# Kernel optimization log

Measured on AMD Instinct MI355X. Metric: run time of the kernel, lower is better.

The kernel has to match this reference:

```python
import jax, jax.numpy as jnp
import numpy as np

B, T, D, H = 1024, 256, 128, 64

def setup_inputs() -> dict:
    key = jax.random.key(0)
    ks = jax.random.split(key, 9)
    s = 1.0 / np.sqrt(H)  # PyTorch LSTM init scale
    x = jax.random.normal(ks[0], (B, T, D), dtype=jnp.float32)
    W_ih = jax.random.uniform(ks[1], (4 * H, D), dtype=jnp.float32, minval=-s, maxval=s)
    W_hh = jax.random.uniform(ks[2], (4 * H, H), dtype=jnp.float32, minval=-s, maxval=s)
    b_ih = jax.random.uniform(ks[3], (4 * H,), dtype=jnp.float32, minval=-s, maxval=s)
    b_hh = jax.random.uniform(ks[4], (4 * H,), dtype=jnp.float32, minval=-s, maxval=s)
    W1 = jax.random.uniform(ks[5], (32, H), dtype=jnp.float32, minval=-s, maxval=s)
    b1 = jax.random.uniform(ks[6], (32,), dtype=jnp.float32, minval=-s, maxval=s)
    W2 = jax.random.uniform(ks[7], (1, 32), dtype=jnp.float32, minval=-0.18, maxval=0.18)
    b2 = jax.random.uniform(ks[8], (1,), dtype=jnp.float32, minval=-0.18, maxval=0.18)
    return {"x": x, "W_ih": W_ih, "W_hh": W_hh, "b_ih": b_ih, "b_hh": b_hh,
            "W1": W1, "b1": b1, "W2": W2, "b2": b2}

def reference(x, W_ih, W_hh, b_ih, b_hh, W1, b1, W2, b2):
    b = b_ih + b_hh
    # Precompute input-to-hidden projections for all timesteps: [B,T,4H]
    x_proj = jnp.einsum('btd,gd->btg', x, W_ih) + b

    def step(carry, xp_t):
        h, c = carry
        gates = xp_t + h @ W_hh.T  # [B,4H]
        i, f, g, o = jnp.split(gates, 4, axis=-1)  # PyTorch gate order
        i = jax.nn.sigmoid(i)
        f = jax.nn.sigmoid(f)
        g = jnp.tanh(g)
        o = jax.nn.sigmoid(o)
        c = f * c + i * g
        h = o * jnp.tanh(c)
        return (h, c), None

    h0 = jnp.zeros((x.shape[0], H), dtype=x.dtype)
    c0 = jnp.zeros((x.shape[0], H), dtype=x.dtype)
    (h, _), _ = jax.lax.scan(step, (h0, c0), jnp.swapaxes(x_proj, 0, 1))  # scan over T

    y = jax.nn.relu(h @ W1.T + b1)  # [B,32]
    y = jax.nn.sigmoid(y @ W2.T + b2)  # [B,1]
    return y.reshape(-1)
```

## Files before the change

kernel.cpp:

```cpp
#include <hip/hip_runtime.h>
#include <math.h>

constexpr int B_ = 1024;
constexpr int T_ = 256;
constexpr int D_ = 128;
constexpr int H_ = 64;
constexpr int G_ = 256;
constexpr int M_ = B_ * T_;

typedef short     v8s __attribute__((ext_vector_type(8)));
typedef float     v4f __attribute__((ext_vector_type(4)));
typedef _Float16  h2  __attribute__((ext_vector_type(2)));

__device__ __forceinline__ float sigmoidf_(float x) {
    return 1.0f / (1.0f + __expf(-x));
}
__device__ __forceinline__ float tanhf_(float x) {
    return fmaf(2.0f, 1.0f / (1.0f + __expf(-2.0f * x)), -1.0f);
}
__device__ __forceinline__ unsigned short f2bf(float f) {
    unsigned u = __float_as_uint(f);
    u = (u + 0x7fffu + ((u >> 16) & 1u)) >> 16;
    return (unsigned short)u;
}
__device__ __forceinline__ v8s pack8(float4 a, float4 b) {
    v8s r;
    r[0] = (short)f2bf(a.x); r[1] = (short)f2bf(a.y);
    r[2] = (short)f2bf(a.z); r[3] = (short)f2bf(a.w);
    r[4] = (short)f2bf(b.x); r[5] = (short)f2bf(b.y);
    r[6] = (short)f2bf(b.z); r[7] = (short)f2bf(b.w);
    return r;
}
__device__ __forceinline__ unsigned pkh2(float a, float b) {
    h2 v; v[0] = (_Float16)a; v[1] = (_Float16)b;
    return __builtin_bit_cast(unsigned, v);
}
__device__ __forceinline__ float fdot2_(unsigned a, unsigned b, float c) {
#if __has_builtin(__builtin_amdgcn_fdot2)
    return __builtin_amdgcn_fdot2(__builtin_bit_cast(h2, a),
                                  __builtin_bit_cast(h2, b), c, false);
#else
    h2 ha = __builtin_bit_cast(h2, a), hb = __builtin_bit_cast(h2, b);
    return c + (float)ha[0] * (float)hb[0] + (float)ha[1] * (float)hb[1];
#endif
}

__global__ __launch_bounds__(256, 2)
void xproj_f16_kernel(const float* __restrict__ x,
                      const float* __restrict__ W_ih,
                      const float* __restrict__ b_ih,
                      const float* __restrict__ b_hh,
                      unsigned short* __restrict__ xp)
{
    const int tch  = blockIdx.x;
    const int bblk = blockIdx.y;
    const int tid  = threadIdx.x;
    const int wv   = tid >> 6;
    const int lane = tid & 63;
    const int q    = lane >> 4;
    const int ml   = lane & 15;

    __shared__ __align__(16) unsigned short xs[16][136];
    __shared__ __align__(16) unsigned short tbuf[16][272];

    v8s afr[4][4];
    v4f bias[4];
    #pragma unroll
    for (int cls = 0; cls < 4; ++cls) {
        const int gr = (cls * 4 + wv) * 16 + ml;
        #pragma unroll
        for (int ks = 0; ks < 4; ++ks) {
            const float* p = W_ih + (size_t)gr * D_ + ks * 32 + q * 8;
            afr[cls][ks] = pack8(((const float4*)p)[0], ((const float4*)p)[1]);
        }
        #pragma unroll
        for (int r = 0; r < 4; ++r) {
            const int g2 = (cls * 4 + wv) * 16 + q * 4 + r;
            bias[cls][r] = b_ih[g2] + b_hh[g2];
        }
    }

    for (int tl = 0; tl < 16; ++tl) {
        const int t = tch * 16 + tl;

        #pragma unroll
        for (int i = 0; i < 2; ++i) {
            int f4  = tid + i * 256;
            int row = f4 >> 5, c4 = f4 & 31;
            float4 v = ((const float4*)(x + ((size_t)(bblk * 16 + row) * T_
                                             + t) * D_))[c4];
            short4 s;
            s.x = (short)f2bf(v.x); s.y = (short)f2bf(v.y);
            s.z = (short)f2bf(v.z); s.w = (short)f2bf(v.w);
            *(short4*)&xs[row][c4 * 4] = s;
        }
        __syncthreads();

        v4f acc[4];
        #pragma unroll
        for (int cls = 0; cls < 4; ++cls) acc[cls] = bias[cls];
        #pragma unroll
        for (int ks = 0; ks < 4; ++ks) {
            v8s bf = *(const v8s*)&xs[ml][ks * 32 + q * 8];
            #pragma unroll
            for (int cls = 0; cls < 4; ++cls)
                acc[cls] = __builtin_amdgcn_mfma_f32_16x16x32_bf16(
                    afr[cls][ks], bf, acc[cls], 0, 0, 0);
        }

        #pragma unroll
        for (int cls = 0; cls < 4; ++cls) {
            uint2 pk;
            pk.x = pkh2(acc[cls][0], acc[cls][1]);
            pk.y = pkh2(acc[cls][2], acc[cls][3]);
            *(uint2*)&tbuf[ml][cls * 64 + wv * 16 + q * 4] = pk;
        }
        __syncthreads();

        {
            const int br = tid >> 4, seg = tid & 15;
            uint4 r0 = *(const uint4*)&tbuf[br][seg * 16];
            uint4 r1 = *(const uint4*)&tbuf[br][seg * 16 + 8];
            unsigned short* orow = xp + ((size_t)(bblk * 16 + br) * T_ + t) * G_
                                      + seg * 16;
            *(uint4*)orow       = r0;
            *(uint4*)(orow + 8) = r1;
        }
    }
}

__global__ __launch_bounds__(256, 4)
void rec_dot2_kernel(const unsigned short* __restrict__ xp,
                     const float* __restrict__ W_hh,
                     const float* __restrict__ W1,
                     const float* __restrict__ b1,
                     const float* __restrict__ W2,
                     const float* __restrict__ b2,
                     float* __restrict__ out)
{
    const int b   = blockIdx.x;
    const int g   = threadIdx.x;
    const int cls = g >> 6;

    __shared__ __align__(16) unsigned hbuf[2][32];
    __shared__ float gates[G_];
    __shared__ float hf[H_];
    __shared__ float ys[32];

    uint4 wp[8];
    #pragma unroll
    for (int k8 = 0; k8 < 8; ++k8) {
        const float* p = W_hh + (size_t)g * H_ + k8 * 8;
        float4 v0 = ((const float4*)p)[0];
        float4 v1 = ((const float4*)p)[1];
        wp[k8].x = pkh2(v0.x, v0.y);
        wp[k8].y = pkh2(v0.z, v0.w);
        wp[k8].z = pkh2(v1.x, v1.y);
        wp[k8].w = pkh2(v1.z, v1.w);
    }

    if (g < 32) hbuf[0][g] = 0u;
    float c = 0.0f, hval = 0.0f;

    const unsigned short* __restrict__ xrow = xp + (size_t)b * T_ * G_ + g;
    unsigned short xv = xrow[0];
    __syncthreads();

    for (int t = 0; t < T_; ++t) {
        const int par = t & 1;
        unsigned short xn = xrow[(size_t)((t + 1 < T_) ? t + 1 : T_ - 1) * G_];

        float a0 = 0.f, a1 = 0.f, a2 = 0.f, a3 = 0.f;
        const uint4* hb = (const uint4*)hbuf[par];
        #pragma unroll
        for (int k8 = 0; k8 < 8; ++k8) {
            uint4 hv = hb[k8];
            a0 = fdot2_(wp[k8].x, hv.x, a0);
            a1 = fdot2_(wp[k8].y, hv.y, a1);
            a2 = fdot2_(wp[k8].z, hv.z, a2);
            a3 = fdot2_(wp[k8].w, hv.w, a3);
        }
        float pre = (float)__builtin_bit_cast(_Float16, xv)
                  + ((a0 + a1) + (a2 + a3));
        gates[g] = (cls == 2) ? tanhf_(pre) : sigmoidf_(pre);
        __syncthreads();

        if (g < H_) {
            float gi = gates[g];
            float gf = gates[H_ + g];
            float gg = gates[2 * H_ + g];
            float go = gates[3 * H_ + g];
            c    = fmaf(gf, c, gi * gg);
            hval = go * tanhf_(c);
            ((_Float16*)hbuf[1 - par])[g] = (_Float16)hval;
        }
        __syncthreads();
        xv = xn;
    }

    if (g < H_) hf[g] = hval;
    __syncthreads();
    if (g < 32) {
        float acc = b1[g];
        const float4* w1r = (const float4*)(W1 + (size_t)g * H_);
        #pragma unroll
        for (int k4 = 0; k4 < 16; ++k4) {
            float4 h4 = *(const float4*)&hf[k4 * 4];
            float4 w4 = w1r[k4];
            acc = fmaf(w4.x, h4.x, acc); acc = fmaf(w4.y, h4.y, acc);
            acc = fmaf(w4.z, h4.z, acc); acc = fmaf(w4.w, h4.w, acc);
        }
        ys[g] = fmaxf(acc, 0.0f);
    }
    __syncthreads();
    if (g == 0) {
        float acc = b2[0];
        #pragma unroll
        for (int j = 0; j < 32; ++j) acc = fmaf(W2[j], ys[j], acc);
        out[b] = sigmoidf_(acc);
    }
}

__global__ __launch_bounds__(256, 2)
void lstm_fused_kernel(const float* __restrict__ x,
                       const float* __restrict__ W_ih,
                       const float* __restrict__ W_hh,
                       const float* __restrict__ b_ih,
                       const float* __restrict__ b_hh,
                       const float* __restrict__ W1,
                       const float* __restrict__ b1,
                       const float* __restrict__ W2,
                       const float* __restrict__ b2,
                       float* __restrict__ out)
{
    const int b = blockIdx.x;
    const int g = threadIdx.x;

    __shared__ __align__(16) float xs[D_];
    __shared__ __align__(16) float hs[H_];
    __shared__ __align__(16) float gts[G_];
    __shared__ __align__(16) float yss[32];

    float wih[D_];
    float whhr[H_];
    {
        const float4* wr = (const float4*)(W_ih + (size_t)g * D_);
        #pragma unroll
        for (int k = 0; k < D_ / 4; ++k) {
            float4 v = wr[k];
            wih[4*k+0] = v.x; wih[4*k+1] = v.y;
            wih[4*k+2] = v.z; wih[4*k+3] = v.w;
        }
    }
    {
        const float4* wr = (const float4*)(W_hh + (size_t)g * H_);
        #pragma unroll
        for (int k = 0; k < H_ / 4; ++k) {
            float4 v = wr[k];
            whhr[4*k+0] = v.x; whhr[4*k+1] = v.y;
            whhr[4*k+2] = v.z; whhr[4*k+3] = v.w;
        }
    }
    const float bg  = b_ih[g] + b_hh[g];
    const int   cls = g >> 6;

    float c = 0.0f;
    if (g < H_) hs[g] = 0.0f;

    const float* __restrict__ xrow = x + (size_t)b * T_ * D_;

    for (int t = 0; t < T_; ++t) {
        if (g < D_) xs[g] = xrow[(size_t)t * D_ + g];
        __syncthreads();

        float a0 = bg, a1 = 0.f, a2 = 0.f, a3 = 0.f;
        const float4* xs4 = (const float4*)xs;
        #pragma unroll
        for (int k = 0; k < D_ / 4; ++k) {
            float4 v = xs4[k];
            a0 = fmaf(wih[4*k+0], v.x, a0);
            a1 = fmaf(wih[4*k+1], v.y, a1);
            a2 = fmaf(wih[4*k+2], v.z, a2);
            a3 = fmaf(wih[4*k+3], v.w, a3);
        }
        const float4* hs4 = (const float4*)hs;
        #pragma unroll
        for (int k = 0; k < H_ / 4; ++k) {
            float4 v = hs4[k];
            a0 = fmaf(whhr[4*k+0], v.x, a0);
            a1 = fmaf(whhr[4*k+1], v.y, a1);
            a2 = fmaf(whhr[4*k+2], v.z, a2);
            a3 = fmaf(whhr[4*k+3], v.w, a3);
        }
        float acc = (a0 + a1) + (a2 + a3);
        gts[g] = (cls == 2) ? tanhf_(acc) : sigmoidf_(acc);
        __syncthreads();

        if (g < H_) {
            float gi = gts[g];
            float gf = gts[H_ + g];
            float gg = gts[2 * H_ + g];
            float go = gts[3 * H_ + g];
            c = fmaf(gf, c, gi * gg);
            hs[g] = go * tanhf_(c);
        }
    }
    __syncthreads();

    if (g < 32) {
        float acc = b1[g];
        const float* w1r = W1 + g * H_;
        #pragma unroll
        for (int k = 0; k < H_; ++k) acc = fmaf(w1r[k], hs[k], acc);
        yss[g] = fmaxf(acc, 0.0f);
    }
    __syncthreads();
    if (g == 0) {
        float acc = b2[0];
        #pragma unroll
        for (int k = 0; k < 32; ++k) acc = fmaf(W2[k], yss[k], acc);
        out[b] = sigmoidf_(acc);
    }
}

extern "C" void kernel_launch(void* const* d_in, const int* in_sizes, int n_in,
                              void* d_out, int out_size, void* d_ws, size_t ws_size,
                              hipStream_t stream) {
    const float* x    = (const float*)d_in[0];
    const float* W_ih = (const float*)d_in[1];
    const float* W_hh = (const float*)d_in[2];
    const float* b_ih = (const float*)d_in[3];
    const float* b_hh = (const float*)d_in[4];
    const float* W1   = (const float*)d_in[5];
    const float* b1   = (const float*)d_in[6];
    const float* W2   = (const float*)d_in[7];
    const float* b2   = (const float*)d_in[8];
    float* out = (float*)d_out;

    const size_t xp_bytes = (size_t)M_ * G_ * sizeof(unsigned short);

    if (ws_size >= xp_bytes) {
        unsigned short* xp = (unsigned short*)d_ws;
        xproj_f16_kernel<<<dim3(16, 64), dim3(256), 0, stream>>>(
            x, W_ih, b_ih, b_hh, xp);
        rec_dot2_kernel<<<dim3(B_), dim3(256), 0, stream>>>(
            xp, W_hh, W1, b1, W2, b2, out);
    } else {
        lstm_fused_kernel<<<dim3(B_), dim3(256), 0, stream>>>(
            x, W_ih, W_hh, b_ih, b_hh, W1, b1, W2, b2, out);
    }
}
```

Baseline: 405.4 us.

## Run LSTM recurrence in a single wavefront per batch row, removing block barriers

The recurrent kernel now uses one 64-lane wavefront per batch element. Each lane computes all four gates for its hidden unit, holding four rows of W_hh packed as fp16 in registers. This removes the shared gate buffer and the two __syncthreads per timestep, which are replaced by an LDS waitcnt inside the single wave. In exchange each lane does four times the dot-product work per step, and register pressure rises enough to cut occupancy. The design also leans on lockstep execution within the wave for the shared h exchange.

```diff
diff --git a/kernel.cpp b/kernel.cpp
--- a/kernel.cpp
+++ b/kernel.cpp
@@ -129,8 +129,8 @@
     }
 }
 
-__global__ __launch_bounds__(256, 4)
-void rec_dot2_kernel(const unsigned short* __restrict__ xp,
+__global__ __launch_bounds__(64, 1)
+void rec_wave_kernel(const unsigned short* __restrict__ xp,
                      const float* __restrict__ W_hh,
                      const float* __restrict__ W1,
                      const float* __restrict__ b1,
@@ -138,71 +138,81 @@
                      const float* __restrict__ b2,
                      float* __restrict__ out)
 {
-    const int b   = blockIdx.x;
-    const int g   = threadIdx.x;
-    const int cls = g >> 6;
-
-    __shared__ __align__(16) unsigned hbuf[2][32];
-    __shared__ float gates[G_];
+    const int b    = blockIdx.x;
+    const int lane = threadIdx.x;
+
+    __shared__ __align__(16) unsigned hb[2][32];
     __shared__ float hf[H_];
     __shared__ float ys[32];
 
-    uint4 wp[8];
+    uint4 wp[4][8];
     #pragma unroll
-    for (int k8 = 0; k8 < 8; ++k8) {
-        const float* p = W_hh + (size_t)g * H_ + k8 * 8;
-        float4 v0 = ((const float4*)p)[0];
-        float4 v1 = ((const float4*)p)[1];
-        wp[k8].x = pkh2(v0.x, v0.y);
-        wp[k8].y = pkh2(v0.z, v0.w);
-        wp[k8].z = pkh2(v1.x, v1.y);
-        wp[k8].w = pkh2(v1.z, v1.w);
-    }
-
-    if (g < 32) hbuf[0][g] = 0u;
+    for (int r = 0; r < 4; ++r) {
+        const float* p = W_hh + (size_t)(r * H_ * 4 + lane) * H_ / 4;
+        p = W_hh + (size_t)(r * 64 + lane) * H_;
+        #pragma unroll
+        for (int k8 = 0; k8 < 8; ++k8) {
+            float4 v0 = ((const float4*)(p + k8 * 8))[0];
+            float4 v1 = ((const float4*)(p + k8 * 8))[1];
+            wp[r][k8].x = pkh2(v0.x, v0.y);
+            wp[r][k8].y = pkh2(v0.z, v0.w);
+            wp[r][k8].z = pkh2(v1.x, v1.y);
+            wp[r][k8].w = pkh2(v1.z, v1.w);
+        }
+    }
+
+    if (lane < 32) { hb[0][lane] = 0u; hb[1][lane] = 0u; }
     float c = 0.0f, hval = 0.0f;
 
-    const unsigned short* __restrict__ xrow = xp + (size_t)b * T_ * G_ + g;
-    unsigned short xv = xrow[0];
+    const unsigned short* __restrict__ xptr = xp + (size_t)b * T_ * G_ + lane;
+    unsigned short xv0 = xptr[0],   xv1 = xptr[64];
+    unsigned short xv2 = xptr[128], xv3 = xptr[192];
     __syncthreads();
 
     for (int t = 0; t < T_; ++t) {
+        const unsigned short* xnp =
+            xptr + (size_t)((t + 1 < T_) ? t + 1 : T_ - 1) * G_;
+        unsigned short xn0 = xnp[0],   xn1 = xnp[64];
+        unsigned short xn2 = xnp[128], xn3 = xnp[192];
+
         const int par = t & 1;
-        unsigned short xn = xrow[(size_t)((t + 1 < T_) ? t + 1 : T_ - 1) * G_];
-
-        float a0 = 0.f, a1 = 0.f, a2 = 0.f, a3 = 0.f;
-        const uint4* hb = (const uint4*)hbuf[par];
+        const uint4* hb4 = (const uint4*)hb[par];
+        float a0[4] = {0.f, 0.f, 0.f, 0.f};
+        float a1[4] = {0.f, 0.f, 0.f, 0.f};
         #pragma unroll
         for (int k8 = 0; k8 < 8; ++k8) {
-            uint4 hv = hb[k8];
-            a0 = fdot2_(wp[k8].x, hv.x, a0);
-            a1 = fdot2_(wp[k8].y, hv.y, a1);
-            a2 = fdot2_(wp[k8].z, hv.z, a2);
-            a3 = fdot2_(wp[k8].w, hv.w, a3);
-        }
-        float pre = (float)__builtin_bit_cast(_Float16, xv)
-                  + ((a0 + a1) + (a2 + a3));
-        gates[g] = (cls == 2) ? tanhf_(pre) : sigmoidf_(pre);
-        __syncthreads();
-
-        if (g < H_) {
-            float gi = gates[g];
-            float gf = gates[H_ + g];
-            float gg = gates[2 * H_ + g];
-            float go = gates[3 * H_ + g];
-            c    = fmaf(gf, c, gi * gg);
-            hval = go * tanhf_(c);
-            ((_Float16*)hbuf[1 - par])[g] = (_Float16)hval;
-        }
-        __syncthreads();
-        xv = xn;
-    }
-
-    if (g < H_) hf[g] = hval;
-    __syncthreads();
-    if (g < 32) {
-        float acc = b1[g];
-        const float4* w1r = (const float4*)(W1 + (size_t)g * H_);
+            uint4 hv = hb4[k8];
+            #pragma unroll
+            for (int r = 0; r < 4; ++r) {
+                a0[r] = fdot2_(wp[r][k8].x, hv.x, a0[r]);
+                a1[r] = fdot2_(wp[r][k8].y, hv.y, a1[r]);
+                a0[r] = fdot2_(wp[r][k8].z, hv.z, a0[r]);
+                a1[r] = fdot2_(wp[r][k8].w, hv.w, a1[r]);
+            }
+        }
+        float pre0 = (float)__builtin_bit_cast(_Float16, xv0) + (a0[0] + a1[0]);
+        float pre1 = (float)__builtin_bit_cast(_Float16, xv1) + (a0[1] + a1[1]);
+        float pre2 = (float)__builtin_bit_cast(_Float16, xv2) + (a0[2] + a1[2]);
+        float pre3 = (float)__builtin_bit_cast(_Float16, xv3) + (a0[3] + a1[3]);
+
+        float gi = sigmoidf_(pre0);
+        float gf = sigmoidf_(pre1);
+        float gg = tanhf_(pre2);
+        float go = sigmoidf_(pre3);
+        c    = fmaf(gf, c, gi * gg);
+        hval = go * tanhf_(c);
+
+        ((_Float16*)hb[par ^ 1])[lane] = (_Float16)hval;
+        asm volatile("s_waitcnt lgkmcnt(0)" ::: "memory");
+
+        xv0 = xn0; xv1 = xn1; xv2 = xn2; xv3 = xn3;
+    }
+
+    hf[lane] = hval;
+    __syncthreads();
+    if (lane < 32) {
+        float acc = b1[lane];
+        const float4* w1r = (const float4*)(W1 + (size_t)lane * H_);
         #pragma unroll
         for (int k4 = 0; k4 < 16; ++k4) {
             float4 h4 = *(const float4*)&hf[k4 * 4];
@@ -210,10 +220,10 @@
             acc = fmaf(w4.x, h4.x, acc); acc = fmaf(w4.y, h4.y, acc);
             acc = fmaf(w4.z, h4.z, acc); acc = fmaf(w4.w, h4.w, acc);
         }
-        ys[g] = fmaxf(acc, 0.0f);
-    }
-    __syncthreads();
-    if (g == 0) {
+        ys[lane] = fmaxf(acc, 0.0f);
+    }
+    __syncthreads();
+    if (lane == 0) {
         float acc = b2[0];
         #pragma unroll
         for (int j = 0; j < 32; ++j) acc = fmaf(W2[j], ys[j], acc);
@@ -343,7 +353,7 @@
         unsigned short* xp = (unsigned short*)d_ws;
         xproj_f16_kernel<<<dim3(16, 64), dim3(256), 0, stream>>>(
             x, W_ih, b_ih, b_hh, xp);
-        rec_dot2_kernel<<<dim3(B_), dim3(256), 0, stream>>>(
+        rec_wave_kernel<<<dim3(B_), dim3(64), 0, stream>>>(
             xp, W_hh, W1, b1, W2, b2, out);
     } else {
         lstm_fused_kernel<<<dim3(B_), dim3(256), 0, stream>>>(
```

New measurement: 383.1 us. 1.06x faster.
